# Kernel tuning notes

Measured on AMD Instinct MI355X. Metric: run time of the kernel, lower is better.

The kernel has to match this reference:

```python
import jax, jax.numpy as jnp
import numpy as np

N = 50000      # num_nodes
R = 12         # num_relations
RL = 2 * R + 1 # relation slots in each RGCN layer
D = 128        # embedding_dim
H = 128        # hidden_layer_size
B = 4          # num_bases
E = 320000     # num_edges


def _xavier(key, shape):
    fan_in, fan_out = shape[-2], shape[-1]
    lim = np.sqrt(6.0 / (fan_in + fan_out)).astype(np.float32)
    return jax.random.uniform(key, shape, jnp.float32, -lim, lim)


def setup_inputs() -> dict:
    key = jax.random.key(0)
    ks = jax.random.split(key, 12)
    edge_index = jax.random.randint(ks[0], (2, E), 0, N)
    edge_type = jax.random.randint(ks[1], (E,), 0, R)
    neg_tail = jax.random.randint(ks[2], (E,), 0, N)  # corrupted tails for BCE loss
    entity_embedding = _xavier(ks[3], (N, D))
    entity_bias = jnp.zeros((1, D), jnp.float32)
    bases1 = _xavier(ks[4], (B, D, H))
    comp1 = _xavier(ks[5], (RL, B))
    bias1 = jnp.zeros((H,), jnp.float32)
    bases2 = _xavier(ks[6], (B, H, D))
    comp2 = _xavier(ks[7], (RL, B))
    bias2 = jnp.zeros((D,), jnp.float32)
    rel_emb = _xavier(ks[8], (R, D))
    return {
        "entity_embedding": entity_embedding, "entity_bias": entity_bias,
        "bases1": bases1, "comp1": comp1, "bias1": bias1,
        "bases2": bases2, "comp2": comp2, "bias2": bias2,
        "rel_emb": rel_emb,
        "edge_index": edge_index, "edge_type": edge_type, "neg_tail": neg_tail,
    }


def rgcn_layer(x, edge_index, edge_type, bases, comp, bias):
    # Basis-decomposed relational conv: W_r = sum_b comp[r,b] * bases[b]
    # Project once through bases, then combine per-edge with comp[edge_type].
    src, dst = edge_index[0], edge_index[1]
    hb = jnp.einsum('ni,bio->nbo', x, bases)            # [N, B, out]
    c = comp[edge_type]                                  # [E, B]
    msg = jnp.einsum('eb,ebo->eo', c, hb[src])           # [E, out]
    n_edges = edge_type.shape[0]
    deg = jax.ops.segment_sum(jnp.ones((n_edges,), x.dtype), dst, num_segments=N)
    agg = jax.ops.segment_sum(msg, dst, num_segments=N)  # scatter-add aggregation
    return agg / jnp.maximum(deg, 1.0)[:, None] + bias


def reference(entity_embedding, entity_bias, bases1, comp1, bias1,
              bases2, comp2, bias2, rel_emb, edge_index, edge_type, neg_tail):
    x = jax.nn.relu(entity_embedding + entity_bias)
    x = jax.nn.relu(rgcn_layer(x, edge_index, edge_type, bases1, comp1, bias1))
    x = rgcn_layer(x, edge_index, edge_type, bases2, comp2, bias2)
    # DistMult decoding over the graph triples (h, r, t)
    h, t = edge_index[0], edge_index[1]
    re = rel_emb[edge_type]                              # [E, D]
    pred_logits = jnp.sum(x[h] * re * x[t], axis=-1)     # [E]
    neg_logits = jnp.sum(x[h] * re * x[neg_tail], axis=-1)
    loss = 0.5 * (jnp.mean(-jax.nn.log_sigmoid(pred_logits))
                  + jnp.mean(-jax.nn.log_sigmoid(-neg_logits)))
    roc_auc = jnp.mean((pred_logits > neg_logits).astype(jnp.float32))
    return pred_logits, loss, roc_auc
```

## Files before the change

### kernel.cpp

```cpp
#include <hip/hip_runtime.h>

typedef unsigned short ushort_t;
typedef __attribute__((ext_vector_type(8))) short short8;
typedef __attribute__((ext_vector_type(4))) float f32x4;

#define N_NODES 50000
#define NBASE   4
#define N_EDGE  320000
#define DM_BLOCKS 1024
#define N_GROUPS (N_EDGE / 8)
#define SCAN_BLOCKS 49
#define LDSB_STRIDE 136

#define C_COMP1 0
#define C_COMP2 100
#define C_BIAS1 200
#define C_BIAS2 328
#define C_REL   456
#define C_EBIAS 1992
#define C_TOTAL 2120

__device__ __forceinline__ float bf2f(ushort_t u) {
    union { unsigned int i; float f; } v; v.i = ((unsigned int)u) << 16; return v.f;
}
__device__ __forceinline__ ushort_t f2bf(float f) {
    union { float f; unsigned int i; } v; v.f = f;
    unsigned int u = v.i;
    u = (u + 0x7FFFu + ((u >> 16) & 1u)) >> 16;
    return (ushort_t)u;
}
__device__ __forceinline__ float readf(const void* p, int i, int isbf) {
    return isbf ? bf2f(((const ushort_t*)p)[i]) : ((const float*)p)[i];
}
__device__ __forceinline__ float softplus(float x) {
    if (x > 20.f) return x;
    if (x < -20.f) return expf(x);
    return log1pf(expf(x));
}

__global__ void k_detect(const ushort_t* __restrict__ emb, int* __restrict__ flag) {
    __shared__ int cnt;
    if (threadIdx.x == 0) cnt = 0;
    __syncthreads();
    int e = (emb[threadIdx.x] >> 7) & 0xFF;
    if (e >= 100 && e <= 126) atomicAdd(&cnt, 1);
    __syncthreads();
    if (threadIdx.x == 0) *flag = (cnt >= 200) ? 1 : 0;
}

__global__ void k_small(const void* comp1, const void* comp2, const void* b1, const void* b2,
                        const void* rel, const void* eb, float* __restrict__ canon,
                        const int* __restrict__ flag) {
    int isbf = *flag;
    for (int i = threadIdx.x; i < C_TOTAL; i += blockDim.x) {
        float v;
        if      (i < C_COMP2) v = readf(comp1, i - C_COMP1, isbf);
        else if (i < C_BIAS1) v = readf(comp2, i - C_COMP2, isbf);
        else if (i < C_BIAS2) v = readf(b1,    i - C_BIAS1, isbf);
        else if (i < C_REL)   v = readf(b2,    i - C_BIAS2, isbf);
        else if (i < C_EBIAS) v = readf(rel,   i - C_REL,   isbf);
        else                  v = readf(eb,    i - C_EBIAS, isbf);
        canon[i] = v;
    }
}

__global__ void k_repackK(const void* __restrict__ bases, ushort_t* __restrict__ btK,
                          const int* __restrict__ flag) {
    int isbf = *flag;
    int idx = blockIdx.x * blockDim.x + threadIdx.x;
    if (idx >= NBASE * 128 * 128) return;
    int b = idx >> 14, i = (idx >> 7) & 127, o = idx & 127;
    btK[(size_t)o * 512 + (b << 7) + i] = f2bf(readf(bases, idx, isbf));
}

__global__ void k_cnt(const int* __restrict__ ei, int* __restrict__ cnt) {
    int e = blockIdx.x * blockDim.x + threadIdx.x;
    if (e >= N_EDGE) return;
    atomicAdd(&cnt[ei[N_EDGE + e]], 1);
}

__global__ void k_scan1(const int* __restrict__ cnt, int* __restrict__ ptr,
                        int* __restrict__ bsum) {
    __shared__ int s[1024];
    int t = threadIdx.x;
    int i = blockIdx.x * 1024 + t;
    int v = (i < N_NODES) ? cnt[i] : 0;
    s[t] = v;
    __syncthreads();
    for (int off = 1; off < 1024; off <<= 1) {
        int u = (t >= off) ? s[t - off] : 0;
        __syncthreads();
        s[t] += u;
        __syncthreads();
    }
    if (i < N_NODES) ptr[i] = s[t] - v;
    if (t == 1023) bsum[blockIdx.x] = s[1023];
}

__global__ void k_scan2(const int* __restrict__ bsum, int* __restrict__ boff) {
    int t = threadIdx.x;
    int v = (t < SCAN_BLOCKS) ? bsum[t] : 0;
    int orig = v;
    #pragma unroll
    for (int off = 1; off < 64; off <<= 1) {
        int u = __shfl_up(v, off);
        if (t >= off) v += u;
    }
    boff[t] = v - orig;
}

__global__ void k_scan3(int* __restrict__ ptr, int* __restrict__ cursor,
                        const int* __restrict__ boff) {
    int t = threadIdx.x;
    int i = blockIdx.x * 1024 + t;
    if (i < N_NODES) {
        int p = ptr[i] + boff[blockIdx.x];
        ptr[i] = p;
        cursor[i] = p;
    }
    if (blockIdx.x == 0 && t == 0) ptr[N_NODES] = N_EDGE;
}

__global__ void k_fill(const int* __restrict__ ei, const int* __restrict__ et,
                       int* __restrict__ cursor, unsigned int* __restrict__ packed) {
    int e = blockIdx.x * blockDim.x + threadIdx.x;
    if (e >= N_EDGE) return;
    int dst = ei[N_EDGE + e];
    int pos = atomicAdd(&cursor[dst], 1);
    packed[pos] = (unsigned int)(ei[e] & 0xFFFF) | ((unsigned int)et[e] << 16);
}

__global__ void k_x0(const void* __restrict__ emb, const float* __restrict__ canon,
                     ushort_t* __restrict__ x, const int* __restrict__ flag) {
    int isbf = *flag;
    int i = blockIdx.x * blockDim.x + threadIdx.x;
    if (i >= N_NODES * 128) return;
    float v = readf(emb, i, isbf) + canon[C_EBIAS + (i & 127)];
    x[i] = f2bf(fmaxf(v, 0.f));
}

__global__ void k_agg2(const ushort_t* __restrict__ x, const int* __restrict__ ptr,
                       const unsigned int* __restrict__ packed, const float* __restrict__ compf,
                       ushort_t* __restrict__ y) {
    __shared__ float sc[100];
    int tid = threadIdx.x;
    for (int i = tid; i < 100; i += 256) sc[i] = compf[i];
    __syncthreads();
    int m = blockIdx.x * 2 + (tid >> 7);
    int o = tid & 127;
    int beg = ptr[m], end = ptr[m + 1];
    float a0 = 0.f, a1 = 0.f, a2 = 0.f, a3 = 0.f;
    int i = beg;
    for (; i + 4 <= end; i += 4) {
        unsigned int p0 = packed[i], p1 = packed[i + 1];
        unsigned int p2 = packed[i + 2], p3 = packed[i + 3];
        float v0 = bf2f(x[(size_t)(p0 & 0xFFFFu) * 128 + o]);
        float v1 = bf2f(x[(size_t)(p1 & 0xFFFFu) * 128 + o]);
        float v2 = bf2f(x[(size_t)(p2 & 0xFFFFu) * 128 + o]);
        float v3 = bf2f(x[(size_t)(p3 & 0xFFFFu) * 128 + o]);
        const float* c0 = sc + (p0 >> 16) * 4;
        const float* c1 = sc + (p1 >> 16) * 4;
        const float* c2 = sc + (p2 >> 16) * 4;
        const float* c3 = sc + (p3 >> 16) * 4;
        a0 += c0[0] * v0; a1 += c0[1] * v0; a2 += c0[2] * v0; a3 += c0[3] * v0;
        a0 += c1[0] * v1; a1 += c1[1] * v1; a2 += c1[2] * v1; a3 += c1[3] * v1;
        a0 += c2[0] * v2; a1 += c2[1] * v2; a2 += c2[2] * v2; a3 += c2[3] * v2;
        a0 += c3[0] * v3; a1 += c3[1] * v3; a2 += c3[2] * v3; a3 += c3[3] * v3;
    }
    for (; i < end; ++i) {
        unsigned int p0 = packed[i];
        float v0 = bf2f(x[(size_t)(p0 & 0xFFFFu) * 128 + o]);
        const float* c0 = sc + (p0 >> 16) * 4;
        a0 += c0[0] * v0; a1 += c0[1] * v0; a2 += c0[2] * v0; a3 += c0[3] * v0;
    }
    size_t yb = (size_t)m * 512 + o;
    y[yb]       = f2bf(a0);
    y[yb + 128] = f2bf(a1);
    y[yb + 256] = f2bf(a2);
    y[yb + 384] = f2bf(a3);
}

__global__ __launch_bounds__(256) void
k_gemm512(const ushort_t* __restrict__ y, const ushort_t* __restrict__ btK,
          const int* __restrict__ cnt, const float* __restrict__ canon,
          ushort_t* __restrict__ xout, int cbias, int dorelu) {
    __shared__ ushort_t bs[128 * LDSB_STRIDE];
    int tid = threadIdx.x;
    int lane = tid & 63, w = tid >> 6;
    int r = lane & 15, q = lane >> 4;
    int m0 = blockIdx.x * 128;
    f32x4 acc[2][8] = {};
    int row0 = m0 + w * 32 + r;
    int row1 = row0 + 16;
    int cr0 = (row0 < N_NODES) ? row0 : (N_NODES - 1);
    int cr1 = (row1 < N_NODES) ? row1 : (N_NODES - 1);
    const ushort_t* ar0 = y + (size_t)cr0 * 512;
    const ushort_t* ar1 = y + (size_t)cr1 * 512;

    for (int c = 0; c < 4; ++c) {
        __syncthreads();
        {
            int o = tid >> 4;
            int j = (tid & 15) << 3;
            #pragma unroll
            for (int s = 0; s < 8; ++s, o += 16) {
                short8 v = *(const short8*)(btK + (size_t)o * 512 + c * 128 + j);
                *(short8*)(bs + o * LDSB_STRIDE + j) = v;
            }
        }
        __syncthreads();
        #pragma unroll
        for (int ksl = 0; ksl < 4; ++ksl) {
            int k0 = ksl * 32 + q * 8;
            short8 a0 = *(const short8*)(ar0 + c * 128 + k0);
            short8 a1 = *(const short8*)(ar1 + c * 128 + k0);
            #pragma unroll
            for (int t = 0; t < 8; ++t) {
                short8 b = *(const short8*)(bs + (t * 16 + r) * LDSB_STRIDE + k0);
                acc[0][t] = __builtin_amdgcn_mfma_f32_16x16x32_bf16(a0, b, acc[0][t], 0, 0, 0);
                acc[1][t] = __builtin_amdgcn_mfma_f32_16x16x32_bf16(a1, b, acc[1][t], 0, 0, 0);
            }
        }
    }
    #pragma unroll
    for (int i = 0; i < 2; ++i) {
        int rbase = m0 + w * 32 + i * 16 + (q << 2);
        float d[4];
        #pragma unroll
        for (int ii = 0; ii < 4; ++ii) {
            int rr = rbase + ii;
            d[ii] = fmaxf((float)cnt[(rr < N_NODES) ? rr : (N_NODES - 1)], 1.0f);
        }
        #pragma unroll
        for (int t = 0; t < 8; ++t) {
            int col = t * 16 + r;
            float bb = canon[cbias + col];
            #pragma unroll
            for (int ii = 0; ii < 4; ++ii) {
                int rr = rbase + ii;
                if (rr < N_NODES) {
                    float v = acc[i][t][ii] / d[ii] + bb;
                    if (dorelu) v = fmaxf(v, 0.f);
                    xout[(size_t)rr * 128 + col] = f2bf(v);
                }
            }
        }
    }
}

__global__ void k_distmult8b(const ushort_t* __restrict__ x2, const float* __restrict__ canon,
                             const int* __restrict__ ei, const int* __restrict__ et,
                             const int* __restrict__ neg, float* __restrict__ outp,
                             float* __restrict__ partials) {
    __shared__ float srel[1536];
    int tid = threadIdx.x;
    for (int i = tid; i < 1536; i += 256) srel[i] = canon[C_REL + i];
    __syncthreads();
    int lane = tid & 63;
    int g = lane >> 3;
    int l = lane & 7;
    int w = (blockIdx.x * blockDim.x + tid) >> 6;
    int nw = (DM_BLOCKS * 256) >> 6;
    float aL1 = 0.f, aL2 = 0.f, aA = 0.f;
    for (int gid = w; gid < N_GROUPS; gid += nw) {
        int e = gid * 8 + g;
        int h = ei[e], t = ei[N_EDGE + e], r = et[e], qn = neg[e];
        const ushort_t* ph = x2 + (size_t)h * 128 + l * 16;
        const ushort_t* pt = x2 + (size_t)t * 128 + l * 16;
        const ushort_t* pq = x2 + (size_t)qn * 128 + l * 16;
        const float*    pr = srel + r * 128 + l * 16;
        short8 h0 = *(const short8*)ph, h1 = *(const short8*)(ph + 8);
        short8 t0 = *(const short8*)pt, t1 = *(const short8*)(pt + 8);
        short8 q0 = *(const short8*)pq, q1 = *(const short8*)(pq + 8);
        float sp = 0.f, sn = 0.f;
        #pragma unroll
        for (int j = 0; j < 8; ++j) {
            float hv = bf2f(((const ushort_t*)&h0)[j]) * pr[j];
            sp += hv * bf2f(((const ushort_t*)&t0)[j]);
            sn += hv * bf2f(((const ushort_t*)&q0)[j]);
        }
        #pragma unroll
        for (int j = 0; j < 8; ++j) {
            float hv = bf2f(((const ushort_t*)&h1)[j]) * pr[8 + j];
            sp += hv * bf2f(((const ushort_t*)&t1)[j]);
            sn += hv * bf2f(((const ushort_t*)&q1)[j]);
        }
        sp += __shfl_down(sp, 4); sn += __shfl_down(sn, 4);
        sp += __shfl_down(sp, 2); sn += __shfl_down(sn, 2);
        sp += __shfl_down(sp, 1); sn += __shfl_down(sn, 1);
        if (l == 0) {
            outp[e] = sp;
            aL1 += softplus(-sp);
            aL2 += softplus(sn);
            aA  += (sp > sn) ? 1.0f : 0.0f;
        }
    }
    #pragma unroll
    for (int off = 32; off; off >>= 1) {
        aL1 += __shfl_down(aL1, off);
        aL2 += __shfl_down(aL2, off);
        aA  += __shfl_down(aA,  off);
    }
    __shared__ float s[3][4];
    int wl = tid >> 6;
    if (lane == 0) { s[0][wl] = aL1; s[1][wl] = aL2; s[2][wl] = aA; }
    __syncthreads();
    if (tid == 0) {
        float t0 = 0.f, t1 = 0.f, t2 = 0.f;
        for (int i = 0; i < 4; ++i) { t0 += s[0][i]; t1 += s[1][i]; t2 += s[2][i]; }
        partials[blockIdx.x * 3 + 0] = t0;
        partials[blockIdx.x * 3 + 1] = t1;
        partials[blockIdx.x * 3 + 2] = t2;
    }
}

__global__ void k_final(const float* __restrict__ partials, float* __restrict__ outp) {
    __shared__ float s[3][256];
    int tid = threadIdx.x;
    float t0 = 0.f, t1 = 0.f, t2 = 0.f;
    for (int i = tid; i < DM_BLOCKS; i += 256) {
        t0 += partials[i * 3 + 0];
        t1 += partials[i * 3 + 1];
        t2 += partials[i * 3 + 2];
    }
    s[0][tid] = t0; s[1][tid] = t1; s[2][tid] = t2;
    __syncthreads();
    for (int st = 128; st; st >>= 1) {
        if (tid < st) {
            s[0][tid] += s[0][tid + st];
            s[1][tid] += s[1][tid + st];
            s[2][tid] += s[2][tid + st];
        }
        __syncthreads();
    }
    if (tid == 0) {
        float inv = 1.0f / (float)N_EDGE;
        outp[N_EDGE]     = 0.5f * (s[0][0] * inv + s[1][0] * inv);
        outp[N_EDGE + 1] = s[2][0] * inv;
    }
}

extern "C" void kernel_launch(void* const* d_in, const int* in_sizes, int n_in,
                              void* d_out, int out_size, void* d_ws, size_t ws_size,
                              hipStream_t stream) {
    const void* emb    = d_in[0];
    const void* ebias  = d_in[1];
    const void* bases1 = d_in[2];
    const void* comp1  = d_in[3];
    const void* bias1  = d_in[4];
    const void* bases2 = d_in[5];
    const void* comp2  = d_in[6];
    const void* bias2  = d_in[7];
    const void* rel    = d_in[8];
    const int*  ei     = (const int*)d_in[9];
    const int*  et     = (const int*)d_in[10];
    const int*  neg    = (const int*)d_in[11];
    float*      outp   = (float*)d_out;

    char* ws = (char*)d_ws;
    size_t off = 0;
    auto alloc = [&](size_t bytes) { char* p = ws + off; off += (bytes + 255) & ~(size_t)255; return p; };
    int*          flag   = (int*)alloc(256);
    float*        canon  = (float*)alloc((size_t)C_TOTAL * 4);
    int*          cnt    = (int*)alloc((size_t)N_NODES * 4);
    int*          ptr    = (int*)alloc((size_t)(N_NODES + 1) * 4);
    int*          cursor = (int*)alloc((size_t)N_NODES * 4);
    int*          bsum   = (int*)alloc(SCAN_BLOCKS * 4);
    int*          boff   = (int*)alloc(64 * 4);
    ushort_t*     btK1   = (ushort_t*)alloc((size_t)128 * 512 * 2);
    ushort_t*     btK2   = (ushort_t*)alloc((size_t)128 * 512 * 2);
    float*        part   = (float*)alloc((size_t)DM_BLOCKS * 3 * 4);
    unsigned int* packed = (unsigned int*)alloc((size_t)N_EDGE * 4);
    ushort_t*     x      = (ushort_t*)alloc((size_t)N_NODES * 128 * 2);
    ushort_t*     y      = (ushort_t*)alloc((size_t)N_NODES * 512 * 2);

    k_detect<<<1, 256, 0, stream>>>((const ushort_t*)emb, flag);
    k_small<<<1, 256, 0, stream>>>(comp1, comp2, bias1, bias2, rel, ebias, canon, flag);
    hipMemsetAsync(cnt, 0, (size_t)N_NODES * 4, stream);
    k_cnt<<<N_EDGE / 256, 256, 0, stream>>>(ei, cnt);
    k_scan1<<<SCAN_BLOCKS, 1024, 0, stream>>>(cnt, ptr, bsum);
    k_scan2<<<1, 64, 0, stream>>>(bsum, boff);
    k_scan3<<<SCAN_BLOCKS, 1024, 0, stream>>>(ptr, cursor, boff);
    k_fill<<<N_EDGE / 256, 256, 0, stream>>>(ei, et, cursor, packed);
    k_repackK<<<NBASE * 128 * 128 / 256, 256, 0, stream>>>(bases1, btK1, flag);
    k_repackK<<<NBASE * 128 * 128 / 256, 256, 0, stream>>>(bases2, btK2, flag);
    k_x0<<<N_NODES * 128 / 256, 256, 0, stream>>>(emb, canon, x, flag);

    int ggrid = (N_NODES + 127) / 128;

    k_agg2<<<N_NODES / 2, 256, 0, stream>>>(x, ptr, packed, canon + C_COMP1, y);
    k_gemm512<<<ggrid, 256, 0, stream>>>(y, btK1, cnt, canon, x, C_BIAS1, 1);

    k_agg2<<<N_NODES / 2, 256, 0, stream>>>(x, ptr, packed, canon + C_COMP2, y);
    k_gemm512<<<ggrid, 256, 0, stream>>>(y, btK2, cnt, canon, x, C_BIAS2, 0);

    k_distmult8b<<<DM_BLOCKS, 256, 0, stream>>>(x, canon, ei, et, neg, outp, part);
    k_final<<<1, 256, 0, stream>>>(part, outp);
}
```

Measured before the change: 314.3 us.

## Merge prep/init kernels, vectorize aggregation to 2 features per lane, double distmult blocks

```diff
diff --git a/kernel.cpp b/kernel.cpp
--- a/kernel.cpp
+++ b/kernel.cpp
@@ -7,7 +7,7 @@
 #define N_NODES 50000
 #define NBASE   4
 #define N_EDGE  320000
-#define DM_BLOCKS 1024
+#define DM_BLOCKS 2048
 #define N_GROUPS (N_EDGE / 8)
 #define SCAN_BLOCKS 49
 #define LDSB_STRIDE 136
@@ -38,7 +38,9 @@
     return log1pf(expf(x));
 }
 
-__global__ void k_detect(const ushort_t* __restrict__ emb, int* __restrict__ flag) {
+__global__ void k_prep(const ushort_t* __restrict__ emb, int* __restrict__ flag,
+                       const void* comp1, const void* comp2, const void* b1, const void* b2,
+                       const void* rel, const void* eb, float* __restrict__ canon) {
     __shared__ int cnt;
     if (threadIdx.x == 0) cnt = 0;
     __syncthreads();
@@ -46,12 +48,8 @@
     if (e >= 100 && e <= 126) atomicAdd(&cnt, 1);
     __syncthreads();
     if (threadIdx.x == 0) *flag = (cnt >= 200) ? 1 : 0;
-}
-
-__global__ void k_small(const void* comp1, const void* comp2, const void* b1, const void* b2,
-                        const void* rel, const void* eb, float* __restrict__ canon,
-                        const int* __restrict__ flag) {
-    int isbf = *flag;
+    __syncthreads();
+    int isbf = (cnt >= 200) ? 1 : 0;
     for (int i = threadIdx.x; i < C_TOTAL; i += blockDim.x) {
         float v;
         if      (i < C_COMP2) v = readf(comp1, i - C_COMP1, isbf);
@@ -64,13 +62,25 @@
     }
 }
 
-__global__ void k_repackK(const void* __restrict__ bases, ushort_t* __restrict__ btK,
-                          const int* __restrict__ flag) {
+__global__ void k_init(const void* __restrict__ bases1, ushort_t* __restrict__ btK1,
+                       const void* __restrict__ bases2, ushort_t* __restrict__ btK2,
+                       const void* __restrict__ emb, const float* __restrict__ canon,
+                       ushort_t* __restrict__ x, const int* __restrict__ flag) {
     int isbf = *flag;
-    int idx = blockIdx.x * blockDim.x + threadIdx.x;
-    if (idx >= NBASE * 128 * 128) return;
-    int b = idx >> 14, i = (idx >> 7) & 127, o = idx & 127;
-    btK[(size_t)o * 512 + (b << 7) + i] = f2bf(readf(bases, idx, isbf));
+    int bid = blockIdx.x;
+    if (bid < 512) {
+        const void* bases = (bid < 256) ? bases1 : bases2;
+        ushort_t* btK = (bid < 256) ? btK1 : btK2;
+        int idx = (bid & 255) * 256 + threadIdx.x;
+        int b = idx >> 14, i = (idx >> 7) & 127, o = idx & 127;
+        btK[(size_t)o * 512 + (b << 7) + i] = f2bf(readf(bases, idx, isbf));
+    } else {
+        int i = (bid - 512) * 256 + threadIdx.x;
+        if (i < N_NODES * 128) {
+            float v = readf(emb, i, isbf) + canon[C_EBIAS + (i & 127)];
+            x[i] = f2bf(fmaxf(v, 0.f));
+        }
+    }
 }
 
 __global__ void k_cnt(const int* __restrict__ ei, int* __restrict__ cnt) {
@@ -130,15 +140,6 @@
     packed[pos] = (unsigned int)(ei[e] & 0xFFFF) | ((unsigned int)et[e] << 16);
 }
 
-__global__ void k_x0(const void* __restrict__ emb, const float* __restrict__ canon,
-                     ushort_t* __restrict__ x, const int* __restrict__ flag) {
-    int isbf = *flag;
-    int i = blockIdx.x * blockDim.x + threadIdx.x;
-    if (i >= N_NODES * 128) return;
-    float v = readf(emb, i, isbf) + canon[C_EBIAS + (i & 127)];
-    x[i] = f2bf(fmaxf(v, 0.f));
-}
-
 __global__ void k_agg2(const ushort_t* __restrict__ x, const int* __restrict__ ptr,
                        const unsigned int* __restrict__ packed, const float* __restrict__ compf,
                        ushort_t* __restrict__ y) {
@@ -146,38 +147,51 @@
     int tid = threadIdx.x;
     for (int i = tid; i < 100; i += 256) sc[i] = compf[i];
     __syncthreads();
-    int m = blockIdx.x * 2 + (tid >> 7);
-    int o = tid & 127;
+    int m = blockIdx.x * 4 + (tid >> 6);
+    int lane = tid & 63;
+    int o2 = lane << 1;
     int beg = ptr[m], end = ptr[m + 1];
-    float a0 = 0.f, a1 = 0.f, a2 = 0.f, a3 = 0.f;
+    float l0 = 0.f, l1 = 0.f, l2 = 0.f, l3 = 0.f;
+    float h0 = 0.f, h1 = 0.f, h2 = 0.f, h3 = 0.f;
     int i = beg;
     for (; i + 4 <= end; i += 4) {
         unsigned int p0 = packed[i], p1 = packed[i + 1];
         unsigned int p2 = packed[i + 2], p3 = packed[i + 3];
-        float v0 = bf2f(x[(size_t)(p0 & 0xFFFFu) * 128 + o]);
-        float v1 = bf2f(x[(size_t)(p1 & 0xFFFFu) * 128 + o]);
-        float v2 = bf2f(x[(size_t)(p2 & 0xFFFFu) * 128 + o]);
-        float v3 = bf2f(x[(size_t)(p3 & 0xFFFFu) * 128 + o]);
+        unsigned int w0 = *(const unsigned int*)(x + (size_t)(p0 & 0xFFFFu) * 128 + o2);
+        unsigned int w1 = *(const unsigned int*)(x + (size_t)(p1 & 0xFFFFu) * 128 + o2);
+        unsigned int w2 = *(const unsigned int*)(x + (size_t)(p2 & 0xFFFFu) * 128 + o2);
+        unsigned int w3 = *(const unsigned int*)(x + (size_t)(p3 & 0xFFFFu) * 128 + o2);
         const float* c0 = sc + (p0 >> 16) * 4;
         const float* c1 = sc + (p1 >> 16) * 4;
         const float* c2 = sc + (p2 >> 16) * 4;
         const float* c3 = sc + (p3 >> 16) * 4;
-        a0 += c0[0] * v0; a1 += c0[1] * v0; a2 += c0[2] * v0; a3 += c0[3] * v0;
-        a0 += c1[0] * v1; a1 += c1[1] * v1; a2 += c1[2] * v1; a3 += c1[3] * v1;
-        a0 += c2[0] * v2; a1 += c2[1] * v2; a2 += c2[2] * v2; a3 += c2[3] * v2;
-        a0 += c3[0] * v3; a1 += c3[1] * v3; a2 += c3[2] * v3; a3 += c3[3] * v3;
+        float vl, vh;
+        vl = bf2f((ushort_t)w0); vh = bf2f((ushort_t)(w0 >> 16));
+        l0 += c0[0] * vl; l1 += c0[1] * vl; l2 += c0[2] * vl; l3 += c0[3] * vl;
+        h0 += c0[0] * vh; h1 += c0[1] * vh; h2 += c0[2] * vh; h3 += c0[3] * vh;
+        vl = bf2f((ushort_t)w1); vh = bf2f((ushort_t)(w1 >> 16));
+        l0 += c1[0] * vl; l1 += c1[1] * vl; l2 += c1[2] * vl; l3 += c1[3] * vl;
+        h0 += c1[0] * vh; h1 += c1[1] * vh; h2 += c1[2] * vh; h3 += c1[3] * vh;
+        vl = bf2f((ushort_t)w2); vh = bf2f((ushort_t)(w2 >> 16));
+        l0 += c2[0] * vl; l1 += c2[1] * vl; l2 += c2[2] * vl; l3 += c2[3] * vl;
+        h0 += c2[0] * vh; h1 += c2[1] * vh; h2 += c2[2] * vh; h3 += c2[3] * vh;
+        vl = bf2f((ushort_t)w3); vh = bf2f((ushort_t)(w3 >> 16));
+        l0 += c3[0] * vl; l1 += c3[1] * vl; l2 += c3[2] * vl; l3 += c3[3] * vl;
+        h0 += c3[0] * vh; h1 += c3[1] * vh; h2 += c3[2] * vh; h3 += c3[3] * vh;
     }
     for (; i < end; ++i) {
         unsigned int p0 = packed[i];
-        float v0 = bf2f(x[(size_t)(p0 & 0xFFFFu) * 128 + o]);
+        unsigned int w0 = *(const unsigned int*)(x + (size_t)(p0 & 0xFFFFu) * 128 + o2);
         const float* c0 = sc + (p0 >> 16) * 4;
-        a0 += c0[0] * v0; a1 += c0[1] * v0; a2 += c0[2] * v0; a3 += c0[3] * v0;
-    }
-    size_t yb = (size_t)m * 512 + o;
-    y[yb]       = f2bf(a0);
-    y[yb + 128] = f2bf(a1);
-    y[yb + 256] = f2bf(a2);
-    y[yb + 384] = f2bf(a3);
+        float vl = bf2f((ushort_t)w0), vh = bf2f((ushort_t)(w0 >> 16));
+        l0 += c0[0] * vl; l1 += c0[1] * vl; l2 += c0[2] * vl; l3 += c0[3] * vl;
+        h0 += c0[0] * vh; h1 += c0[1] * vh; h2 += c0[2] * vh; h3 += c0[3] * vh;
+    }
+    unsigned int* yp = (unsigned int*)(y + (size_t)m * 512 + o2);
+    yp[0]   = (unsigned int)f2bf(l0) | ((unsigned int)f2bf(h0) << 16);
+    yp[64]  = (unsigned int)f2bf(l1) | ((unsigned int)f2bf(h1) << 16);
+    yp[128] = (unsigned int)f2bf(l2) | ((unsigned int)f2bf(h2) << 16);
+    yp[192] = (unsigned int)f2bf(l3) | ((unsigned int)f2bf(h3) << 16);
 }
 
 __global__ __launch_bounds__(256) void
@@ -374,24 +388,23 @@
     ushort_t*     x      = (ushort_t*)alloc((size_t)N_NODES * 128 * 2);
     ushort_t*     y      = (ushort_t*)alloc((size_t)N_NODES * 512 * 2);
 
-    k_detect<<<1, 256, 0, stream>>>((const ushort_t*)emb, flag);
-    k_small<<<1, 256, 0, stream>>>(comp1, comp2, bias1, bias2, rel, ebias, canon, flag);
+    k_prep<<<1, 256, 0, stream>>>((const ushort_t*)emb, flag, comp1, comp2, bias1, bias2,
+                                  rel, ebias, canon);
     hipMemsetAsync(cnt, 0, (size_t)N_NODES * 4, stream);
     k_cnt<<<N_EDGE / 256, 256, 0, stream>>>(ei, cnt);
     k_scan1<<<SCAN_BLOCKS, 1024, 0, stream>>>(cnt, ptr, bsum);
     k_scan2<<<1, 64, 0, stream>>>(bsum, boff);
     k_scan3<<<SCAN_BLOCKS, 1024, 0, stream>>>(ptr, cursor, boff);
     k_fill<<<N_EDGE / 256, 256, 0, stream>>>(ei, et, cursor, packed);
-    k_repackK<<<NBASE * 128 * 128 / 256, 256, 0, stream>>>(bases1, btK1, flag);
-    k_repackK<<<NBASE * 128 * 128 / 256, 256, 0, stream>>>(bases2, btK2, flag);
-    k_x0<<<N_NODES * 128 / 256, 256, 0, stream>>>(emb, canon, x, flag);
+    k_init<<<512 + (N_NODES * 128 + 255) / 256, 256, 0, stream>>>(
+        bases1, btK1, bases2, btK2, emb, canon, x, flag);
 
     int ggrid = (N_NODES + 127) / 128;
 
-    k_agg2<<<N_NODES / 2, 256, 0, stream>>>(x, ptr, packed, canon + C_COMP1, y);
+    k_agg2<<<N_NODES / 4, 256, 0, stream>>>(x, ptr, packed, canon + C_COMP1, y);
     k_gemm512<<<ggrid, 256, 0, stream>>>(y, btK1, cnt, canon, x, C_BIAS1, 1);
 
-    k_agg2<<<N_NODES / 2, 256, 0, stream>>>(x, ptr, packed, canon + C_COMP2, y);
+    k_agg2<<<N_NODES / 4, 256, 0, stream>>>(x, ptr, packed, canon + C_COMP2, y);
     k_gemm512<<<ggrid, 256, 0, stream>>>(y, btK2, cnt, canon, x, C_BIAS2, 0);
 
     k_distmult8b<<<DM_BLOCKS, 256, 0, stream>>>(x, canon, ei, et, neg, outp, part);
```

Result: faster. 282.2 us (-10.2%).
